# Kernel tuning notes

Measured on AMD Instinct MI355X. Metric: run time of the kernel, lower is better.

Reference implementation:

```python
import jax, jax.numpy as jnp
import numpy as np

TEMPERATURE = 0.1
WEIGHT = 5.0
IS_SYMMETRIC = True


def setup_inputs() -> dict:
    key = jax.random.key(0)
    k1, k2, k3, k4, k5 = jax.random.split(key, 5)
    B, D = 2048, 128
    z_hat = jax.random.normal(k1, (1, B, D), dtype=jnp.float32)  # unused except batch size
    mu_x = jax.random.normal(k2, (B, D), dtype=jnp.float32)
    sigma_x = jax.random.uniform(k3, (B, D), minval=0.5, maxval=1.5, dtype=jnp.float32)
    mu_p = jax.random.normal(k4, (B, D), dtype=jnp.float32)
    sigma_p = jax.random.uniform(k5, (B, D), minval=0.5, maxval=1.5, dtype=jnp.float32)
    return {"z_hat": z_hat, "mu_x": mu_x, "sigma_x": sigma_x, "mu_p": mu_p, "sigma_p": sigma_p}


def _pairwise_kl(mus, sigmas):
    # K[a, b] = KL( N(mu_b, sig_b) || N(mu_a, sig_a) )  (matches torch repeat/repeat_interleave layout)
    D = mus.shape[1]
    var = sigmas * sigmas                      # [N, D]
    inv = 1.0 / var                            # [N, D]
    logdet = jnp.sum(jnp.log(sigmas), axis=1)  # [N]
    tr = jnp.einsum("ad,bd->ab", inv, var)                       # sum_d var_b / var_a
    quad = (jnp.einsum("ad,bd->ab", inv, mus * mus)
            - 2.0 * jnp.einsum("ad,bd->ab", mus * inv, mus)
            + jnp.sum(mus * mus * inv, axis=1)[:, None])         # sum_d (mu_b - mu_a)^2 / var_a
    return logdet[:, None] - logdet[None, :] + 0.5 * (tr + quad) - 0.5 * D


def reference(z_hat, mu_x, sigma_x, mu_p, sigma_p):
    B = mu_x.shape[0]
    N = 2 * B
    mus = jnp.concatenate([mu_x, mu_p], axis=0)       # [N, D]
    sigmas = jnp.concatenate([sigma_x, sigma_p], axis=0)

    logits = -_pairwise_kl(mus, sigmas)               # [N, N]
    if IS_SYMMETRIC:
        logits = (logits + logits.T) / 2
    logits = logits / TEMPERATURE

    # is_invariant=True: drop the diagonal -> [N, N-1] (static gather, jit-friendly)
    rows = jnp.arange(N)[:, None]
    cols = jnp.arange(N - 1)[None, :]
    idx = cols + (cols >= rows).astype(cols.dtype)    # skip column == row
    logits = jnp.take_along_axis(logits, jnp.broadcast_to(idx, (N, N - 1)), axis=1)

    n_classes = N - 1
    ar = jnp.arange(B)
    pos_idx = jnp.concatenate([ar + B - 1, ar], axis=0)  # [N]

    # weight != 1 branch: add -log(to_mult) at the positive logit of each row
    to_mult = (n_classes - 1.0 / WEIGHT) / (n_classes - 1)
    to_add = -jnp.log(jnp.asarray(to_mult, logits.dtype))
    logits = logits.at[jnp.arange(N), pos_idx].add(to_add)

    logp = jax.nn.log_softmax(logits, axis=1)
    hat_H_mlz = -jnp.mean(logp[jnp.arange(N), pos_idx])
    return hat_H_mlz
```

## Files before the change

kernel.cpp:

```cpp
#include <hip/hip_runtime.h>
#include <hip/hip_bf16.h>
#include <math.h>

typedef float f32x4 __attribute__((ext_vector_type(4)));
typedef long  i64;

#define B_HALF 2048
#define N_TOT  4096
#define D_DIM  128
#define NGRP   32
#define NBLK   528
#define KSTEPS 8
#define ROWB   512

__device__ unsigned red_done;

__device__ __forceinline__ short pk8(float x, float y) {
  return (short)__builtin_amdgcn_cvt_pk_fp8_f32(x, y, 0, false);
}

__global__ __launch_bounds__(256) void prep_feat(
    const float* __restrict__ mu_x, const float* __restrict__ sigma_x,
    const float* __restrict__ mu_p, const float* __restrict__ sigma_p,
    unsigned char* __restrict__ Gf8, float* __restrict__ a) {
  const int tid = threadIdx.x;
  const int wv = tid >> 6;
  const int ln = tid & 63;
  const int d0 = ln * 2;
  const float SQ2 = 1.41421356237309515f;
#pragma unroll
  for (int rr = 0; rr < 16; rr += 4) {
    const int row = blockIdx.x * 16 + rr + wv;
    const float* mup = (row < B_HALF) ? mu_x : mu_p;
    const float* sgp = (row < B_HALF) ? sigma_x : sigma_p;
    const int gi = row & (B_HALF - 1);
    const float2 m2 = *(const float2*)(mup + gi * D_DIM + d0);
    const float2 s2 = *(const float2*)(sgp + gi * D_DIM + d0);
    float var0 = s2.x * s2.x, inv0 = 1.0f / var0, vm0 = var0 + m2.x * m2.x;
    float var1 = s2.y * s2.y, inv1 = 1.0f / var1, vm1 = var1 + m2.y * m2.y;
    size_t base = (size_t)row * ROWB;
    *(short*)(Gf8 + base + 0   + d0) = pk8(inv0, inv1);
    *(short*)(Gf8 + base + 128 + d0) = pk8(vm0, vm1);
    *(short*)(Gf8 + base + 256 + d0) = pk8(SQ2 * m2.x * inv0, SQ2 * m2.y * inv1);
    *(short*)(Gf8 + base + 384 + d0) = pk8(-SQ2 * m2.x, -SQ2 * m2.y);

    float av = m2.x * m2.x * inv0 + m2.y * m2.y * inv1;
#pragma unroll
    for (int x = 1; x < 64; x <<= 1) av += __shfl_xor(av, x);
    if (ln == 0) a[row] = av;
  }
}

#define GLOAD16(src, dst)                                                     \
  __builtin_amdgcn_global_load_lds(                                           \
      (const __attribute__((address_space(1))) void*)(src),                   \
      (__attribute__((address_space(3))) void*)(dst), 16, 0, 0)

__global__ __launch_bounds__(256, 3) void gemm_lse(
    const unsigned char* __restrict__ Gf8, const float* __restrict__ a,
    float* __restrict__ lsep, float* __restrict__ pos, float to_add) {
  __shared__ char lt[3][128 * 64];
  __shared__ char rt[3][128 * 64];
  __shared__ float2 red[128][2];

  const int sb = (blockIdx.x & 7) * (NBLK / 8) + (blockIdx.x >> 3);
  int rb, cb;
  if (sb < 144) {
    const int k = sb / 36;
    int t = sb - k * 36;
    int i = 0;
    while (t >= 8 - i) { t -= 8 - i; ++i; }
    rb = k * 8 + i;
    cb = k * 8 + i + t;
  } else {
    const int o = (sb - 144) >> 6;
    const int t = (sb - 144) & 63;
    const int k1 = (o < 3) ? 0 : ((o < 5) ? 1 : 2);
    const int k2 = (o < 3) ? (o + 1) : ((o < 5) ? (o - 1) : 3);
    rb = k1 * 8 + (t >> 3);
    cb = k2 * 8 + (t & 7);
  }

  const int tid  = threadIdx.x;
  const int lane = tid & 63;
  const int wave = tid >> 6;
  const int rowBase = rb * 128, colBase = cb * 128;
  const int wr = wave >> 1, wc = wave & 1;
  const int lx = lane & 15;
  const int rq = lane >> 4;

  f32x4 acc[4][4];
#pragma unroll
  for (int m = 0; m < 4; ++m)
#pragma unroll
    for (int n = 0; n < 4; ++n) acc[m][n] = (f32x4){0.f, 0.f, 0.f, 0.f};

  const int sr  = lane >> 2;
  const int scb = (((lane & 3) ^ (sr & 3)) << 4);
  const char* lsrc0 = (const char*)Gf8 + (size_t)rowBase * ROWB;
  const char* rsrc0 = (const char*)Gf8 + (size_t)colBase * ROWB;

#define STAGE(KK)                                                             \
  {                                                                           \
    const int b_ = (KK) % 3;                                                  \
    const char* ls_ = lsrc0 + (KK) * 64;                                      \
    const char* rs_ = rsrc0 + ((KK) ^ 2) * 64;                                \
    _Pragma("unroll")                                                         \
    for (int g = 0; g < 2; ++g) {                                             \
      const int row_ = wave * 32 + g * 16;                                    \
      GLOAD16(ls_ + (size_t)(row_ + sr) * ROWB + scb, &lt[b_][row_ * 64]);    \
      GLOAD16(rs_ + (size_t)(row_ + sr) * ROWB + scb, &rt[b_][row_ * 64]);    \
    }                                                                         \
  }

  STAGE(0)
  STAGE(1)

#pragma unroll
  for (int kk = 0; kk < KSTEPS; ++kk) {
    if (kk < KSTEPS - 1) asm volatile("s_waitcnt vmcnt(4)" ::: "memory");
    else                 asm volatile("s_waitcnt vmcnt(0)" ::: "memory");
    __builtin_amdgcn_s_barrier();
    __builtin_amdgcn_sched_barrier(0);
    if (kk + 2 < KSTEPS) STAGE(kk + 2)
    const int b = kk % 3;
#pragma unroll
    for (int ks = 0; ks < 2; ++ks) {
      i64 af[4], bg[4];
      const int q16 = ks * 2 + (rq >> 1);
      const int sub = (rq & 1) * 8;
#pragma unroll
      for (int m = 0; m < 4; ++m) {
        const int row = wr * 64 + m * 16 + lx;
        af[m] = *(const i64*)(&lt[b][row * 64 + ((q16 ^ (row & 3)) << 4) + sub]);
      }
#pragma unroll
      for (int n = 0; n < 4; ++n) {
        const int row = wc * 64 + n * 16 + lx;
        bg[n] = *(const i64*)(&rt[b][row * 64 + ((q16 ^ (row & 3)) << 4) + sub]);
      }
#pragma unroll
      for (int m = 0; m < 4; ++m)
#pragma unroll
        for (int n = 0; n < 4; ++n)
          acc[m][n] = __builtin_amdgcn_mfma_f32_16x16x32_fp8_fp8(af[m], bg[n], acc[m][n], 0, 0, 0);
    }
  }
#undef STAGE

  const float c0 = 640.0f;
  const float c1 = 2.5f;
  float aR[4][4];
#pragma unroll
  for (int m = 0; m < 4; ++m)
#pragma unroll
    for (int v = 0; v < 4; ++v)
      aR[m][v] = a[rowBase + wr * 64 + m * 16 + rq * 4 + v];
  float aC[4];
#pragma unroll
  for (int n = 0; n < 4; ++n) aC[n] = a[colBase + wc * 64 + n * 16 + lx];

#pragma unroll
  for (int m = 0; m < 4; ++m)
#pragma unroll
    for (int n = 0; n < 4; ++n)
#pragma unroll
      for (int v = 0; v < 4; ++v) {
        int grow = rowBase + wr * 64 + m * 16 + rq * 4 + v;
        int gcol = colBase + wc * 64 + n * 16 + lx;
        float S = c0 - c1 * (acc[m][n][v] + aR[m][v] + aC[n]);
        if (gcol == grow) {
          S = -INFINITY;
        } else if (gcol == (grow ^ B_HALF)) {
          S += to_add;
          pos[grow] = S;
          pos[gcol] = S;
        }
        acc[m][n][v] = S;
      }

#pragma unroll
  for (int m = 0; m < 4; ++m)
#pragma unroll
    for (int v = 0; v < 4; ++v) {
      float pm = -INFINITY;
#pragma unroll
      for (int n = 0; n < 4; ++n) pm = fmaxf(pm, acc[m][n][v]);
#pragma unroll
      for (int x = 1; x < 16; x <<= 1) pm = fmaxf(pm, __shfl_xor(pm, x));
      float ps = 0.f;
#pragma unroll
      for (int n = 0; n < 4; ++n) ps += __expf(acc[m][n][v] - pm);
#pragma unroll
      for (int x = 1; x < 16; x <<= 1) ps += __shfl_xor(ps, x);
      if (lx == 0) red[wr * 64 + m * 16 + rq * 4 + v][wc] = make_float2(pm, ps);
    }
  __syncthreads();
  if (tid < 128) {
    float2 p0 = red[tid][0], p1 = red[tid][1];
    float M = fmaxf(p0.x, p1.x);
    float S = p0.y * __expf(p0.x - M) + p1.y * __expf(p1.x - M);
    lsep[(size_t)(rowBase + tid) * NGRP + cb] = M + logf(S);
  }

  if (rb != cb) {
    __syncthreads();
#pragma unroll
    for (int n = 0; n < 4; ++n) {
      float cm = -INFINITY;
#pragma unroll
      for (int m = 0; m < 4; ++m)
#pragma unroll
        for (int v = 0; v < 4; ++v) cm = fmaxf(cm, acc[m][n][v]);
      cm = fmaxf(cm, __shfl_xor(cm, 16));
      cm = fmaxf(cm, __shfl_xor(cm, 32));
      float cs = 0.f;
#pragma unroll
      for (int m = 0; m < 4; ++m)
#pragma unroll
        for (int v = 0; v < 4; ++v) cs += __expf(acc[m][n][v] - cm);
      cs += __shfl_xor(cs, 16);
      cs += __shfl_xor(cs, 32);
      if (lane < 16) red[wc * 64 + n * 16 + lane][wr] = make_float2(cm, cs);
    }
    __syncthreads();
    if (tid < 128) {
      float2 p0 = red[tid][0], p1 = red[tid][1];
      float M = fmaxf(p0.x, p1.x);
      float S = p0.y * __expf(p0.x - M) + p1.y * __expf(p1.x - M);
      lsep[(size_t)(colBase + tid) * NGRP + rb] = M + logf(S);
    }
  }
}

__global__ __launch_bounds__(256) void reduce_final(
    const float* __restrict__ lsep, const float* __restrict__ pos,
    float* __restrict__ partial, float* __restrict__ out) {
  const int tid = threadIdx.x;
  const int row = blockIdx.x * 256 + tid;
  const float* lp = lsep + (size_t)row * NGRP;
  float M = lp[0];
#pragma unroll
  for (int k = 1; k < NGRP; ++k) M = fmaxf(M, lp[k]);
  float s = 0.f;
#pragma unroll
  for (int k = 0; k < NGRP; ++k) s += __expf(lp[k] - M);
  float contrib = (M + logf(s)) - pos[row];

  __shared__ float fr[256];
  fr[tid] = contrib;
  __syncthreads();
#pragma unroll
  for (int off = 128; off > 0; off >>= 1) {
    if (tid < off) fr[tid] += fr[tid + off];
    __syncthreads();
  }
  if (tid == 0) {
    partial[blockIdx.x] = fr[0];
    unsigned v = __hip_atomic_fetch_add(&red_done, 1u, __ATOMIC_ACQ_REL,
                                        __HIP_MEMORY_SCOPE_AGENT);
    if (v == 15u) {
      float tot = 0.f;
      for (int k = 0; k < 16; ++k) tot += partial[k];
      out[0] = tot * (1.0f / 4096.0f);
      __hip_atomic_store(&red_done, 0u, __ATOMIC_RELAXED,
                         __HIP_MEMORY_SCOPE_AGENT);
    }
  }
}

extern "C" void kernel_launch(void* const* d_in, const int* in_sizes, int n_in,
                              void* d_out, int out_size, void* d_ws, size_t ws_size,
                              hipStream_t stream) {
  const float* mu_x    = (const float*)d_in[1];
  const float* sigma_x = (const float*)d_in[2];
  const float* mu_p    = (const float*)d_in[3];
  const float* sigma_p = (const float*)d_in[4];
  float* out = (float*)d_out;

  float to_add = (float)(-log((4095.0 - 1.0 / 5.0) / 4094.0));

  const size_t featB = (size_t)N_TOT * ROWB;
  char* ws = (char*)d_ws;
  unsigned char* Gf8 = (unsigned char*)(ws);
  float* a       = (float*)(ws + featB);
  float* lsep    = (float*)(ws + featB + 16384);
  float* pos     = (float*)(ws + featB + 16384 + 524288);
  float* partial = (float*)(ws + featB + 16384 + 524288 + 16384);

  prep_feat<<<dim3(256), dim3(256), 0, stream>>>(mu_x, sigma_x, mu_p, sigma_p,
                                                 Gf8, a);
  gemm_lse<<<dim3(NBLK), dim3(256), 0, stream>>>(Gf8, a, lsep, pos, to_add);
  reduce_final<<<dim3(16), dim3(256), 0, stream>>>(lsep, pos, partial, out);
}
```

Measured before the change: 37.15 us.

## Load GEMM fragments directly from global with chunk-major FP8 feature layout

The FP8 feature matrix is rewritten in a chunk-major layout (8 chunks of 64 bytes per row, each a contiguous [N,64] slab), and the GEMM kernel drops the LDS triple-buffered global_load_lds pipeline. Each lane now reads its 8-byte MFMA operands straight from global memory. This removes barriers, LDS traffic and shared memory use, which may let more blocks run per CU. In exchange the operand reuse across waves now depends on L1/L2 caches, and the loads are small, not explicitly pipelined, and exposed to global latency.

New measurement: 46.91 us. +26.3%, slower.

```diff
diff --git a/kernel.cpp b/kernel.cpp
--- a/kernel.cpp
+++ b/kernel.cpp
@@ -10,8 +10,8 @@
 #define D_DIM  128
 #define NGRP   32
 #define NBLK   528
-#define KSTEPS 8
-#define ROWB   512
+#define NCHUNK 8
+#define CHUNKB (N_TOT * 64)
 
 __device__ unsigned red_done;
 
@@ -22,11 +22,13 @@
 __global__ __launch_bounds__(256) void prep_feat(
     const float* __restrict__ mu_x, const float* __restrict__ sigma_x,
     const float* __restrict__ mu_p, const float* __restrict__ sigma_p,
-    unsigned char* __restrict__ Gf8, float* __restrict__ a) {
+    unsigned char* __restrict__ GfT, float* __restrict__ a) {
   const int tid = threadIdx.x;
   const int wv = tid >> 6;
   const int ln = tid & 63;
   const int d0 = ln * 2;
+  const int hi = d0 >> 6;
+  const int off = d0 & 63;
   const float SQ2 = 1.41421356237309515f;
 #pragma unroll
   for (int rr = 0; rr < 16; rr += 4) {
@@ -38,11 +40,11 @@
     const float2 s2 = *(const float2*)(sgp + gi * D_DIM + d0);
     float var0 = s2.x * s2.x, inv0 = 1.0f / var0, vm0 = var0 + m2.x * m2.x;
     float var1 = s2.y * s2.y, inv1 = 1.0f / var1, vm1 = var1 + m2.y * m2.y;
-    size_t base = (size_t)row * ROWB;
-    *(short*)(Gf8 + base + 0   + d0) = pk8(inv0, inv1);
-    *(short*)(Gf8 + base + 128 + d0) = pk8(vm0, vm1);
-    *(short*)(Gf8 + base + 256 + d0) = pk8(SQ2 * m2.x * inv0, SQ2 * m2.y * inv1);
-    *(short*)(Gf8 + base + 384 + d0) = pk8(-SQ2 * m2.x, -SQ2 * m2.y);
+    const size_t rb = (size_t)row * 64 + off;
+    *(short*)(GfT + (size_t)(0 + hi) * CHUNKB + rb) = pk8(inv0, inv1);
+    *(short*)(GfT + (size_t)(2 + hi) * CHUNKB + rb) = pk8(vm0, vm1);
+    *(short*)(GfT + (size_t)(4 + hi) * CHUNKB + rb) = pk8(SQ2 * m2.x * inv0, SQ2 * m2.y * inv1);
+    *(short*)(GfT + (size_t)(6 + hi) * CHUNKB + rb) = pk8(-SQ2 * m2.x, -SQ2 * m2.y);
 
     float av = m2.x * m2.x * inv0 + m2.y * m2.y * inv1;
 #pragma unroll
@@ -51,16 +53,9 @@
   }
 }
 
-#define GLOAD16(src, dst)                                                     \
-  __builtin_amdgcn_global_load_lds(                                           \
-      (const __attribute__((address_space(1))) void*)(src),                   \
-      (__attribute__((address_space(3))) void*)(dst), 16, 0, 0)
-
 __global__ __launch_bounds__(256, 3) void gemm_lse(
-    const unsigned char* __restrict__ Gf8, const float* __restrict__ a,
+    const unsigned char* __restrict__ GfT, const float* __restrict__ a,
     float* __restrict__ lsep, float* __restrict__ pos, float to_add) {
-  __shared__ char lt[3][128 * 64];
-  __shared__ char rt[3][128 * 64];
   __shared__ float2 red[128][2];
 
   const int sb = (blockIdx.x & 7) * (NBLK / 8) + (blockIdx.x >> 3);
@@ -95,50 +90,25 @@
 #pragma unroll
     for (int n = 0; n < 4; ++n) acc[m][n] = (f32x4){0.f, 0.f, 0.f, 0.f};
 
-  const int sr  = lane >> 2;
-  const int scb = (((lane & 3) ^ (sr & 3)) << 4);
-  const char* lsrc0 = (const char*)Gf8 + (size_t)rowBase * ROWB;
-  const char* rsrc0 = (const char*)Gf8 + (size_t)colBase * ROWB;
-
-#define STAGE(KK)                                                             \
-  {                                                                           \
-    const int b_ = (KK) % 3;                                                  \
-    const char* ls_ = lsrc0 + (KK) * 64;                                      \
-    const char* rs_ = rsrc0 + ((KK) ^ 2) * 64;                                \
-    _Pragma("unroll")                                                         \
-    for (int g = 0; g < 2; ++g) {                                             \
-      const int row_ = wave * 32 + g * 16;                                    \
-      GLOAD16(ls_ + (size_t)(row_ + sr) * ROWB + scb, &lt[b_][row_ * 64]);    \
-      GLOAD16(rs_ + (size_t)(row_ + sr) * ROWB + scb, &rt[b_][row_ * 64]);    \
-    }                                                                         \
-  }
-
-  STAGE(0)
-  STAGE(1)
-
-#pragma unroll
-  for (int kk = 0; kk < KSTEPS; ++kk) {
-    if (kk < KSTEPS - 1) asm volatile("s_waitcnt vmcnt(4)" ::: "memory");
-    else                 asm volatile("s_waitcnt vmcnt(0)" ::: "memory");
-    __builtin_amdgcn_s_barrier();
-    __builtin_amdgcn_sched_barrier(0);
-    if (kk + 2 < KSTEPS) STAGE(kk + 2)
-    const int b = kk % 3;
+  const int vlane = lx * 64 + rq * 8;
+  const int voffA = wr * 4096 + vlane;
+  const int voffB = wc * 4096 + vlane;
+
+#pragma unroll
+  for (int kk = 0; kk < NCHUNK; ++kk) {
+    const char* Ak = (const char*)GfT + (size_t)kk * CHUNKB +
+                     (size_t)rowBase * 64 + voffA;
+    const char* Bk = (const char*)GfT + (size_t)(kk ^ 2) * CHUNKB +
+                     (size_t)colBase * 64 + voffB;
 #pragma unroll
     for (int ks = 0; ks < 2; ++ks) {
       i64 af[4], bg[4];
-      const int q16 = ks * 2 + (rq >> 1);
-      const int sub = (rq & 1) * 8;
-#pragma unroll
-      for (int m = 0; m < 4; ++m) {
-        const int row = wr * 64 + m * 16 + lx;
-        af[m] = *(const i64*)(&lt[b][row * 64 + ((q16 ^ (row & 3)) << 4) + sub]);
-      }
-#pragma unroll
-      for (int n = 0; n < 4; ++n) {
-        const int row = wc * 64 + n * 16 + lx;
-        bg[n] = *(const i64*)(&rt[b][row * 64 + ((q16 ^ (row & 3)) << 4) + sub]);
-      }
+#pragma unroll
+      for (int m = 0; m < 4; ++m)
+        af[m] = *(const i64*)(Ak + m * 1024 + ks * 32);
+#pragma unroll
+      for (int n = 0; n < 4; ++n)
+        bg[n] = *(const i64*)(Bk + n * 1024 + ks * 32);
 #pragma unroll
       for (int m = 0; m < 4; ++m)
 #pragma unroll
@@ -146,7 +116,6 @@
           acc[m][n] = __builtin_amdgcn_mfma_f32_16x16x32_fp8_fp8(af[m], bg[n], acc[m][n], 0, 0, 0);
     }
   }
-#undef STAGE
 
   const float c0 = 640.0f;
   const float c1 = 2.5f;
@@ -280,16 +249,17 @@
 
   float to_add = (float)(-log((4095.0 - 1.0 / 5.0) / 4094.0));
 
-  const size_t featB = (size_t)N_TOT * ROWB;
+  const size_t featB = (size_t)NCHUNK * CHUNKB;
   char* ws = (char*)d_ws;
-  unsigned char* Gf8 = (unsigned char*)(ws);
-  float* a       = (float*)(ws + featB);
-  float* lsep    = (float*)(ws + featB + 16384);
-  float* pos     = (float*)(ws + featB + 16384 + 524288);
-  float* partial = (float*)(ws + featB + 16384 + 524288 + 16384);
+  unsigned char* GfT = (unsigned char*)(ws);
+  size_t off = featB;
+  float* a       = (float*)(ws + off); off += 16384;
+  float* lsep    = (float*)(ws + off); off += 524288;
+  float* pos     = (float*)(ws + off); off += 16384;
+  float* partial = (float*)(ws + off); off += 16384;
 
   prep_feat<<<dim3(256), dim3(256), 0, stream>>>(mu_x, sigma_x, mu_p, sigma_p,
-                                                 Gf8, a);
-  gemm_lse<<<dim3(NBLK), dim3(256), 0, stream>>>(Gf8, a, lsep, pos, to_add);
+                                                 GfT, a);
+  gemm_lse<<<dim3(NBLK), dim3(256), 0, stream>>>(GfT, a, lsep, pos, to_add);
   reduce_final<<<dim3(16), dim3(256), 0, stream>>>(lsep, pos, partial, out);
 }
```
